# Kernel optimization log

Measured on AMD Instinct MI355X. Metric: run time of the kernel, lower is better.

Reference implementation:

```python
import jax, jax.numpy as jnp
import numpy as np

L, D, HQ, HKV, HD, P, V, B, S = 4, 2048, 16, 4, 128, 8192, 32000, 2, 1024
THETA, EPS = 500000.0, 1e-5
RATIO = HQ // HKV  # GQA q-to-kv ratio = 4


def rmsnorm(x, w):
    # torch: w * (x * rsqrt(mean(x^2, -1) + eps)) computed in fp32
    x32 = x.astype(jnp.float32)
    n = x32 * jax.lax.rsqrt(jnp.mean(x32 * x32, axis=-1, keepdims=True) + EPS)
    return w * n.astype(x.dtype)


def make_rope(seq_len):
    inv = 1.0 / (THETA ** (jnp.arange(0, HD, 2, dtype=jnp.float32) / HD))  # [HD/2]
    ang = jnp.arange(seq_len, dtype=jnp.float32)[:, None] * inv[None, :]   # [S, HD/2]
    return jnp.cos(ang)[None, :, None, :], jnp.sin(ang)[None, :, None, :]  # [1,S,1,HD/2]


def rope(t, cos, sin):
    # torch code: complex = t[..., :HD/2] + i*t[..., HD/2:], multiply by e^{i*ang},
    # then view_as_real + flatten -> INTERLEAVED (r0,i0,r1,i1,...) output layout.
    h = HD // 2
    r, im = t[..., :h], t[..., h:]
    orr = r * cos - im * sin
    oim = r * sin + im * cos
    return jnp.stack([orr, oim], axis=-1).reshape(t.shape)


def attention(x, wqkv, wo, cos, sin):
    b, s, _ = x.shape
    qkv = x @ wqkv                               # [b,s,D+2*HKV*HD]
    q = qkv[..., :D].reshape(b, s, HQ, HD)
    k = qkv[..., D:D + HKV * HD].reshape(b, s, HKV, HD)
    v = qkv[..., D + HKV * HD:].reshape(b, s, HKV, HD)
    q = rope(q, cos, sin)
    k = rope(k, cos, sin)
    # GQA: repeat_interleave kv heads to match q heads (offset=0 prefill; cache is identity)
    k = jnp.repeat(k, RATIO, axis=2)
    v = jnp.repeat(v, RATIO, axis=2)
    scale = 1.0 / np.sqrt(HD)
    scores = jnp.einsum('bqhd,bkhd->bhqk', q, k) * scale
    causal = jnp.tril(jnp.ones((s, s), dtype=bool))
    scores = jnp.where(causal[None, None], scores, jnp.finfo(scores.dtype).min)
    probs = jax.nn.softmax(scores, axis=-1)
    out = jnp.einsum('bhqk,bkhd->bqhd', probs, v).reshape(b, s, D)
    return out @ wo


def swiglu(x, wgu, wd):
    gu = x @ wgu                                  # [b,s,2P]
    gate, up = gu[..., :P], gu[..., P:]
    return (jax.nn.silu(gate) * up) @ wd


def setup_inputs() -> dict:
    key = jax.random.key(0)
    ks = jax.random.split(key, 8)
    sc = 0.02
    return {
        'tokens': jax.random.randint(ks[0], (B, S), 0, V),
        'emb': jax.random.normal(ks[1], (V, D), jnp.float32) * sc,
        'w_qkv': jax.random.normal(ks[2], (L, D, D + 2 * HKV * HD), jnp.float32) * sc,
        'w_o': jax.random.normal(ks[3], (L, D, D), jnp.float32) * sc,
        'w_gate_up': jax.random.normal(ks[4], (L, D, 2 * P), jnp.float32) * sc,
        'w_down': jax.random.normal(ks[5], (L, P, D), jnp.float32) * sc,
        'ln_attn': jnp.ones((L, D), jnp.float32),
        'ln_ffn': jnp.ones((L, D), jnp.float32),
        'ln_f': jnp.ones((D,), jnp.float32),
        'w_lm': jax.random.normal(ks[6], (D, V), jnp.float32) * sc,
    }


def reference(tokens, emb, w_qkv, w_o, w_gate_up, w_down, ln_attn, ln_ffn, ln_f, w_lm):
    cos, sin = make_rope(S)
    x = emb[tokens]                               # [B,S,D]
    for l in range(L):
        x = x + attention(rmsnorm(x, ln_attn[l]), w_qkv[l], w_o[l], cos, sin)
        x = x + swiglu(rmsnorm(x, ln_ffn[l]), w_gate_up[l], w_down[l])
    return rmsnorm(x, ln_f) @ w_lm                # logits [B,S,V]
```

## Files before the change

kernel.cpp:

```cpp
#include <hip/hip_runtime.h>
#include <hip/hip_bf16.h>
#include <math.h>

#define S_LEN 1024
#define DIM   2048
#define NHQ   16
#define NHKV  4
#define HDIM  128
#define PDIM  8192
#define VOCAB 32000
#define NLAYER 4
#define NROWS (2 * S_LEN)

typedef __attribute__((ext_vector_type(4))) float f32x4;
typedef __attribute__((ext_vector_type(8))) short bf16x8;

__device__ __forceinline__ void gload_lds16(const void* g, void* l) {
  __builtin_amdgcn_global_load_lds(
      (const __attribute__((address_space(1))) unsigned int*)g,
      (__attribute__((address_space(3))) unsigned int*)l, 16, 0, 0);
}

#define FENCE() asm volatile("" ::: "memory")

__global__ __launch_bounds__(256) void k_embed(const int* __restrict__ tokens,
    const float* __restrict__ emb, float* __restrict__ x) {
  int row = blockIdx.x;
  int tok = tokens[row];
  const f32x4* src = (const f32x4*)(emb + (size_t)tok * DIM);
  f32x4* dst = (f32x4*)(x + (size_t)row * DIM);
  for (int i = threadIdx.x; i < DIM / 4; i += 256) dst[i] = src[i];
}

__global__ __launch_bounds__(256) void k_rmsnorm(const float* __restrict__ x,
    const float* __restrict__ w, __hip_bfloat16* __restrict__ out) {
  int row = blockIdx.x;
  const float* xr = x + (size_t)row * DIM;
  float ss = 0.f;
  for (int i = threadIdx.x; i < DIM; i += 256) { float v = xr[i]; ss += v * v; }
  for (int off = 32; off; off >>= 1) ss += __shfl_xor(ss, off);
  __shared__ float wsum[4];
  if ((threadIdx.x & 63) == 0) wsum[threadIdx.x >> 6] = ss;
  __syncthreads();
  float tot = wsum[0] + wsum[1] + wsum[2] + wsum[3];
  float r = rsqrtf(tot / (float)DIM + 1e-5f);
  __hip_bfloat16* orow = out + (size_t)row * DIM;
  for (int i = threadIdx.x; i < DIM; i += 256)
    orow[i] = __float2bfloat16(w[i] * (xr[i] * r));
}

__global__ __launch_bounds__(256) void k_wt(const float* __restrict__ W,
    __hip_bfloat16* __restrict__ WT, int K, int N) {
  __shared__ __hip_bfloat16 t[64][72];
  int k0 = blockIdx.y * 64, n0 = blockIdx.x * 64;
  int r = threadIdx.x >> 4;
  int c4 = (threadIdx.x & 15) * 4;
#pragma unroll
  for (int i = 0; i < 4; ++i) {
    int k = r + i * 16;
    f32x4 v = *(const f32x4*)(W + (size_t)(k0 + k) * N + n0 + c4);
#pragma unroll
    for (int j = 0; j < 4; ++j) t[c4 + j][k] = __float2bfloat16(v[j]);
  }
  __syncthreads();
  int n = threadIdx.x >> 2, kc = (threadIdx.x & 3) * 16;
  bf16x8* dst = (bf16x8*)(WT + (size_t)(n0 + n) * K + k0 + kc);
  dst[0] = *(const bf16x8*)&t[n][kc];
  dst[1] = *(const bf16x8*)&t[n][kc + 8];
}

__global__ __launch_bounds__(256) void k_wt_gu(const float* __restrict__ W,
    __hip_bfloat16* __restrict__ WT, int K, int N) {
  __shared__ __hip_bfloat16 t[64][72];
  int k0 = blockIdx.y * 64, n0 = blockIdx.x * 64;
  int r = threadIdx.x >> 4;
  int c4 = (threadIdx.x & 15) * 4;
  int nblk = (n0 + c4) >> 4;
  int jj   = (n0 + c4) & 15;
  int srcc = ((nblk & 1) ? PDIM : 0) + ((nblk >> 1) << 4) + jj;
#pragma unroll
  for (int i = 0; i < 4; ++i) {
    int k = r + i * 16;
    f32x4 v = *(const f32x4*)(W + (size_t)(k0 + k) * N + srcc);
#pragma unroll
    for (int j = 0; j < 4; ++j) t[c4 + j][k] = __float2bfloat16(v[j]);
  }
  __syncthreads();
  int n = threadIdx.x >> 2, kc = (threadIdx.x & 3) * 16;
  bf16x8* dst = (bf16x8*)(WT + (size_t)(n0 + n) * K + k0 + kc);
  dst[0] = *(const bf16x8*)&t[n][kc];
  dst[1] = *(const bf16x8*)&t[n][kc + 8];
}

template<int EPI>
__global__ __launch_bounds__(512) void k_gemm256(
    const __hip_bfloat16* __restrict__ A, const __hip_bfloat16* __restrict__ BT,
    void* __restrict__ Cv, int M, int N, int K) {
  __shared__ __hip_bfloat16 AsH[4][128][64];
  __shared__ __hip_bfloat16 BsH[4][128][64];
  const int NH = K >> 5;
  int tid = threadIdx.x;
  int bid = blockIdx.x;
  int mt = bid & 7, nt = bid >> 3;
  int bm = mt << 8, bn = nt << 8;
  int wave = tid >> 6, lane = tid & 63;
  int wm = wave >> 2, wn = wave & 3;
  int g = lane >> 4, c = lane & 15;
  f32x4 acc[8][4] = {};

  int pre  = (lane & 7) ^ (lane >> 3);
  int rOff = (lane >> 3) * 2 + (pre >> 2);
  int cOff = (pre & 3) * 8;

  auto stageA = [&](int S, int h) {
#pragma unroll
    for (int rd = 0; rd < 2; ++rd) {
      int seg = rd * 8 + wave;
      gload_lds16(A + (size_t)(bm + seg * 16 + rOff) * K + h * 32 + cOff,
                  &AsH[S][seg * 8 + (lane >> 3)][(lane & 7) * 8]);
    }
  };
  auto stageB = [&](int S, int h) {
#pragma unroll
    for (int rd = 0; rd < 2; ++rd) {
      int seg = rd * 8 + wave;
      gload_lds16(BT + (size_t)(bn + seg * 16 + rOff) * K + h * 32 + cOff,
                  &BsH[S][seg * 8 + (lane >> 3)][(lane & 7) * 8]);
    }
  };

  stageA(0, 0); stageB(0, 0);
  stageA(1, 1); stageB(1, 1);
  stageB(2, 2);
  asm volatile("s_waitcnt vmcnt(6)" ::: "memory");
  __builtin_amdgcn_s_barrier();
  FENCE();

  int lineA = wm * 64 + (c >> 1);
  int lineB = wn * 32 + (c >> 1);
  int slotE = ((((c & 1) << 2) | g) ^ (c >> 1)) * 8;

  for (int H = 0; H < NH; ++H) {
    int S = H & 3;
    bf16x8 af[8], bv[4];
#pragma unroll
    for (int mi = 0; mi < 8; ++mi)
      af[mi] = *(const bf16x8*)&AsH[S][lineA + mi * 8][slotE];
#pragma unroll
    for (int ni = 0; ni < 4; ++ni)
      bv[ni] = *(const bf16x8*)&BsH[S][lineB + ni * 8][slotE];
    FENCE();
    if (H + 2 < NH) stageA((H + 2) & 3, H + 2);
    if (H + 3 < NH) stageB((H + 3) & 3, H + 3);
    if (H + 4 <= NH)      { asm volatile("s_waitcnt vmcnt(6)" ::: "memory"); }
    else if (H + 3 == NH) { asm volatile("s_waitcnt vmcnt(4)" ::: "memory"); }
    else if (H + 2 == NH) { asm volatile("s_waitcnt vmcnt(0)" ::: "memory"); }
    __builtin_amdgcn_s_barrier();
    asm volatile("s_waitcnt lgkmcnt(0)" ::: "memory");
    __builtin_amdgcn_sched_barrier(0);
    __builtin_amdgcn_s_setprio(1);
#pragma unroll
    for (int mi = 0; mi < 8; ++mi)
#pragma unroll
      for (int ni = 0; ni < 4; ++ni)
        acc[mi][ni] = __builtin_amdgcn_mfma_f32_16x16x32_bf16(af[mi], bv[ni], acc[mi][ni], 0, 0, 0);
    __builtin_amdgcn_s_setprio(0);
    FENCE();
    __builtin_amdgcn_s_barrier();
    FENCE();
  }

  float* Cf = (float*)Cv;
  __hip_bfloat16* Cb = (__hip_bfloat16*)Cv;
  int row0 = bm + wm * 128, col0 = bn + wn * 64;
  if (EPI == 3) {
#pragma unroll
    for (int mi = 0; mi < 8; ++mi)
#pragma unroll
      for (int ni = 0; ni < 4; ni += 2)
#pragma unroll
        for (int r = 0; r < 4; ++r) {
          int row = row0 + mi * 16 + g * 4 + r;
          int hcol = ((col0 + ni * 16) >> 1) + c;
          float gate = acc[mi][ni][r], up = acc[mi][ni + 1][r];
          float sv = gate / (1.f + __expf(-gate)) * up;
          Cb[(size_t)row * PDIM + hcol] = __float2bfloat16(sv);
        }
  } else {
#pragma unroll
    for (int mi = 0; mi < 8; ++mi)
#pragma unroll
      for (int ni = 0; ni < 4; ++ni)
#pragma unroll
        for (int r = 0; r < 4; ++r) {
          int row = row0 + mi * 16 + g * 4 + r;
          int col = col0 + ni * 16 + c;
          size_t idx = (size_t)row * N + col;
          if (EPI == 0) Cf[idx] = acc[mi][ni][r];
          else if (EPI == 1) Cf[idx] += acc[mi][ni][r];
          else Cb[idx] = __float2bfloat16(acc[mi][ni][r]);
        }
  }
}

template<int EPI, int KSPLIT = 1>
__global__ __launch_bounds__(256) void k_gemm_bt(
    const __hip_bfloat16* __restrict__ A, const __hip_bfloat16* __restrict__ BT,
    void* __restrict__ Cv, int M, int N, int K) {
  __shared__ __hip_bfloat16 As[2][128][64];
  __shared__ __hip_bfloat16 Bs[2][128][64];
  int nm = M >> 7;
  int bid = blockIdx.x;
  int mt, nt;
  if (nm == 16) {
    int xcd = bid & 7;
    int seq = bid >> 3;
    mt = (xcd << 1) | (seq & 1);
    nt = seq >> 1;
  } else {
    mt = bid % nm;
    nt = bid / nm;
  }
  int bm = mt << 7, bn = nt << 7;
  const int Keff = K / KSPLIT;
  const int kbase = (KSPLIT > 1) ? (int)blockIdx.y * Keff : 0;
  int tid  = threadIdx.x;
  int wave = tid >> 6, lane = tid & 63;
  int wr = (wave >> 1) * 64, wc = (wave & 1) * 64;
  int g = lane >> 4, c = lane & 15;
  f32x4 acc[4][4] = {};

  auto stage = [&](int buf, int k0) {
#pragma unroll
    for (int i = 0; i < 4; ++i) {
      int ci = i * 256 + tid;
      int row = ci >> 3, pc = ci & 7;
      int jl = pc ^ (row & 7);
      gload_lds16(A + (size_t)(bm + row) * K + kbase + k0 + jl * 8, &As[buf][row][pc * 8]);
      gload_lds16(BT + (size_t)(bn + row) * K + kbase + k0 + jl * 8, &Bs[buf][row][pc * 8]);
    }
  };

  int ntiles = Keff >> 6;
  stage(0, 0);
  if (ntiles > 1) stage(1, 64);

  for (int t = 0; t < ntiles; ++t) {
    int cur = t & 1;
    if (t + 1 < ntiles) asm volatile("s_waitcnt vmcnt(8)" ::: "memory");
    else                asm volatile("s_waitcnt vmcnt(0)" ::: "memory");
    __builtin_amdgcn_s_barrier();
    FENCE();
    __builtin_amdgcn_sched_barrier(0);
#pragma unroll
    for (int kk = 0; kk < 2; ++kk) {
      bf16x8 af[4], bv[4];
#pragma unroll
      for (int mi = 0; mi < 4; ++mi) {
        int row = wr + mi * 16 + c;
        int ch = (kk * 4 + g) ^ (row & 7);
        af[mi] = *(const bf16x8*)&As[cur][row][ch * 8];
      }
#pragma unroll
      for (int ni = 0; ni < 4; ++ni) {
        int row = wc + ni * 16 + c;
        int ch = (kk * 4 + g) ^ (row & 7);
        bv[ni] = *(const bf16x8*)&Bs[cur][row][ch * 8];
      }
      __builtin_amdgcn_s_setprio(1);
#pragma unroll
      for (int mi = 0; mi < 4; ++mi)
#pragma unroll
        for (int ni = 0; ni < 4; ++ni)
          acc[mi][ni] = __builtin_amdgcn_mfma_f32_16x16x32_bf16(af[mi], bv[ni], acc[mi][ni], 0, 0, 0);
      __builtin_amdgcn_s_setprio(0);
    }
    FENCE();
    __builtin_amdgcn_s_barrier();
    FENCE();
    if (t + 2 < ntiles) stage(cur, (t + 2) << 6);
  }

  float* Cf = (float*)Cv;
  __hip_bfloat16* Cb = (__hip_bfloat16*)Cv;
#pragma unroll
  for (int mi = 0; mi < 4; ++mi)
#pragma unroll
    for (int ni = 0; ni < 4; ++ni)
#pragma unroll
      for (int r = 0; r < 4; ++r) {
        int row = bm + wr + mi * 16 + g * 4 + r;
        int col = bn + wc + ni * 16 + c;
        size_t idx = (size_t)row * N + col;
        if (EPI == 0) Cf[idx] = acc[mi][ni][r];
        else if (EPI == 1) Cf[idx] += acc[mi][ni][r];
        else if (EPI == 2) Cb[idx] = __float2bfloat16(acc[mi][ni][r]);
        else atomicAdd(&Cf[idx], acc[mi][ni][r]);
      }
}

template<int EPI>
__global__ __launch_bounds__(256) void k_gemm(
    const __hip_bfloat16* __restrict__ A, const float* __restrict__ Bw,
    void* __restrict__ Cv, int M, int N, int K) {
  __shared__ __hip_bfloat16 As[128][32];
  __shared__ __hip_bfloat16 Bs[128][40];
  int tid  = threadIdx.x;
  int bm = blockIdx.y * 128, bn = blockIdx.x * 128;
  int wave = tid >> 6, lane = tid & 63;
  int wr = (wave >> 1) * 64, wc = (wave & 1) * 64;
  int lrow = lane & 15, lk = (lane >> 4) * 8;
  f32x4 acc[4][4] = {};
  for (int k0 = 0; k0 < K; k0 += 32) {
#pragma unroll
    for (int i = 0; i < 2; ++i) {
      int L = i * 256 + tid;
      int row = L >> 2, koff = (L & 3) * 8;
      gload_lds16(A + (size_t)(bm + row) * K + k0 + koff, &As[row][koff]);
    }
#pragma unroll
    for (int i = 0; i < 4; ++i) {
      int L = i * 256 + tid;
      int kk = L >> 5;
      int c4 = (L & 31) * 4;
      f32x4 v = *(const f32x4*)(Bw + (size_t)(k0 + kk) * N + bn + c4);
#pragma unroll
      for (int j = 0; j < 4; ++j) Bs[c4 + j][kk] = __float2bfloat16(v[j]);
    }
    __syncthreads();
    bf16x8 af[4], bfr[4];
#pragma unroll
    for (int mi = 0; mi < 4; ++mi)
      af[mi] = *(const bf16x8*)(&As[wr + mi * 16 + lrow][lk]);
#pragma unroll
    for (int ni = 0; ni < 4; ++ni)
      bfr[ni] = *(const bf16x8*)(&Bs[wc + ni * 16 + lrow][lk]);
#pragma unroll
    for (int mi = 0; mi < 4; ++mi)
#pragma unroll
      for (int ni = 0; ni < 4; ++ni)
        acc[mi][ni] = __builtin_amdgcn_mfma_f32_16x16x32_bf16(af[mi], bfr[ni], acc[mi][ni], 0, 0, 0);
    __syncthreads();
  }
  float* Cf = (float*)Cv;
  __hip_bfloat16* Cb = (__hip_bfloat16*)Cv;
#pragma unroll
  for (int mi = 0; mi < 4; ++mi)
#pragma unroll
    for (int ni = 0; ni < 4; ++ni)
#pragma unroll
      for (int r = 0; r < 4; ++r) {
        int row = bm + wr + mi * 16 + ((lane >> 4) * 4 + r);
        int col = bn + wc + ni * 16 + (lane & 15);
        size_t idx = (size_t)row * N + col;
        if (EPI == 0) Cf[idx] = acc[mi][ni][r];
        else if (EPI == 1) Cf[idx] += acc[mi][ni][r];
        else Cb[idx] = __float2bfloat16(acc[mi][ni][r]);
      }
}

__global__ __launch_bounds__(256) void k_rope(const __hip_bfloat16* __restrict__ qkv,
    __hip_bfloat16* __restrict__ qr, __hip_bfloat16* __restrict__ kr,
    __hip_bfloat16* __restrict__ vt) {
  int rowid = blockIdx.x;
  int b = rowid >> 10, s = rowid & (S_LEN - 1);
  const __hip_bfloat16* src = qkv + (size_t)rowid * 3072;
  const float kInvLog = 0.20503692777f;
  const float scale = 0.08838834764831845f;
  __shared__ float cs[64], sn[64];
  if (threadIdx.x < 64) {
    float inv = expf(-(float)threadIdx.x * kInvLog);
    float a = (float)s * inv;
    sincosf(a, &sn[threadIdx.x], &cs[threadIdx.x]);
  }
  __syncthreads();
  for (int it = threadIdx.x; it < NHQ * 64; it += 256) {
    int h = it >> 6, i = it & 63;
    float re = __bfloat162float(src[h * HDIM + i]);
    float im = __bfloat162float(src[h * HDIM + 64 + i]);
    size_t dst = ((size_t)(b * NHQ + h) * S_LEN + s) * HDIM;
    qr[dst + 2 * i]     = __float2bfloat16((re * cs[i] - im * sn[i]) * scale);
    qr[dst + 2 * i + 1] = __float2bfloat16((re * sn[i] + im * cs[i]) * scale);
  }
  for (int it = threadIdx.x; it < NHKV * 64; it += 256) {
    int h = it >> 6, i = it & 63;
    float re = __bfloat162float(src[DIM + h * HDIM + i]);
    float im = __bfloat162float(src[DIM + h * HDIM + 64 + i]);
    size_t dst = ((size_t)(b * NHKV + h) * S_LEN + s) * HDIM;
    kr[dst + 2 * i]     = __float2bfloat16(re * cs[i] - im * sn[i]);
    kr[dst + 2 * i + 1] = __float2bfloat16(re * sn[i] + im * cs[i]);
  }
  for (int it = threadIdx.x; it < NHKV * HDIM; it += 256) {
    int h = it >> 7, d = it & 127;
    vt[(((size_t)b * NHKV + h) * HDIM + d) * S_LEN + s] = src[DIM + NHKV * HDIM + it];
  }
}

__global__ __launch_bounds__(256) void k_attn_mfma(
    const __hip_bfloat16* __restrict__ Q,
    const __hip_bfloat16* __restrict__ Kc,
    const __hip_bfloat16* __restrict__ VT,
    __hip_bfloat16* __restrict__ O) {
  __shared__ __hip_bfloat16 plds[4][16][40];
  int wave = threadIdx.x >> 6, lane = threadIdx.x & 63;
  int gw = blockIdx.x * 4 + wave;
  int qt = gw & 63;
  int bh = gw >> 6;
  int b = bh >> 4, h = bh & 15;
  int hk = h >> 2;
  int q0 = qt * 16;
  int g = lane >> 4, c = lane & 15;
  const __hip_bfloat16* Qb = Q + ((size_t)bh * S_LEN + q0) * HDIM;
  const __hip_bfloat16* Kb = Kc + (size_t)(b * NHKV + hk) * S_LEN * HDIM;
  const __hip_bfloat16* Vb = VT + (size_t)(b * NHKV + hk) * S_LEN * HDIM;

  bf16x8 qf[4];
#pragma unroll
  for (int cn = 0; cn < 4; ++cn)
    qf[cn] = *(const bf16x8*)(Qb + (size_t)c * HDIM + cn * 32 + g * 8);

  f32x4 po[8] = {};
  float m[4], l[4];
#pragma unroll
  for (int r = 0; r < 4; ++r) { m[r] = -1e30f; l[r] = 0.f; }

  int kvend = q0 + 16;
  for (int kv0 = 0; kv0 < kvend; kv0 += 32) {
    f32x4 s0 = {}, s1 = {};
#pragma unroll
    for (int cn = 0; cn < 4; ++cn) {
      bf16x8 k0f = *(const bf16x8*)(Kb + (size_t)(kv0 + c) * HDIM + cn * 32 + g * 8);
      bf16x8 k1f = *(const bf16x8*)(Kb + (size_t)(kv0 + 16 + c) * HDIM + cn * 32 + g * 8);
      s0 = __builtin_amdgcn_mfma_f32_16x16x32_bf16(qf[cn], k0f, s0, 0, 0, 0);
      s1 = __builtin_amdgcn_mfma_f32_16x16x32_bf16(qf[cn], k1f, s1, 0, 0, 0);
    }
    if (kv0 + 31 > q0) {
#pragma unroll
      for (int r = 0; r < 4; ++r) {
        int qrow = q0 + g * 4 + r;
        if (kv0 + c > qrow)      s0[r] = -1e30f;
        if (kv0 + 16 + c > qrow) s1[r] = -1e30f;
      }
    }
    float rm[4];
#pragma unroll
    for (int r = 0; r < 4; ++r) rm[r] = fmaxf(s0[r], s1[r]);
#pragma unroll
    for (int off = 1; off < 16; off <<= 1)
#pragma unroll
      for (int r = 0; r < 4; ++r) rm[r] = fmaxf(rm[r], __shfl_xor(rm[r], off));
    float p0[4], p1[4], rs[4];
#pragma unroll
    for (int r = 0; r < 4; ++r) {
      float mn = fmaxf(m[r], rm[r]);
      float corr = __expf(m[r] - mn);
      m[r] = mn;
      p0[r] = __expf(s0[r] - mn);
      p1[r] = __expf(s1[r] - mn);
      rs[r] = p0[r] + p1[r];
      l[r] *= corr;
#pragma unroll
      for (int t = 0; t < 8; ++t) po[t][r] *= corr;
    }
#pragma unroll
    for (int off = 1; off < 16; off <<= 1)
#pragma unroll
      for (int r = 0; r < 4; ++r) rs[r] += __shfl_xor(rs[r], off);
#pragma unroll
    for (int r = 0; r < 4; ++r) l[r] += rs[r];
#pragma unroll
    for (int r = 0; r < 4; ++r) {
      plds[wave][g * 4 + r][c]      = __float2bfloat16(p0[r]);
      plds[wave][g * 4 + r][16 + c] = __float2bfloat16(p1[r]);
    }
    bf16x8 pf = *(const bf16x8*)&plds[wave][c][g * 8];
#pragma unroll
    for (int t = 0; t < 8; ++t) {
      bf16x8 vf = *(const bf16x8*)(Vb + (size_t)(t * 16 + c) * S_LEN + kv0 + g * 8);
      po[t] = __builtin_amdgcn_mfma_f32_16x16x32_bf16(pf, vf, po[t], 0, 0, 0);
    }
  }
  float inv[4];
#pragma unroll
  for (int r = 0; r < 4; ++r) inv[r] = 1.f / l[r];
  __hip_bfloat16* ob = O + ((size_t)(b * S_LEN) + q0) * DIM + h * HDIM;
#pragma unroll
  for (int t = 0; t < 8; ++t)
#pragma unroll
    for (int r = 0; r < 4; ++r)
      ob[(size_t)(g * 4 + r) * DIM + t * 16 + c] = __float2bfloat16(po[t][r] * inv[r]);
}

extern "C" void kernel_launch(void* const* d_in, const int* in_sizes, int n_in,
                              void* d_out, int out_size, void* d_ws, size_t ws_size,
                              hipStream_t stream) {
  const int*   tokens    = (const int*)d_in[0];
  const float* emb       = (const float*)d_in[1];
  const float* w_qkv     = (const float*)d_in[2];
  const float* w_o       = (const float*)d_in[3];
  const float* w_gate_up = (const float*)d_in[4];
  const float* w_down    = (const float*)d_in[5];
  const float* ln_attn   = (const float*)d_in[6];
  const float* ln_ffn    = (const float*)d_in[7];
  const float* ln_f      = (const float*)d_in[8];
  const float* w_lm      = (const float*)d_in[9];
  float* out = (float*)d_out;

  char* ws = (char*)d_ws;
  float* x = (float*)ws;                    ws += (size_t)NROWS * DIM * 4;
  __hip_bfloat16* xn = (__hip_bfloat16*)ws; ws += (size_t)NROWS * DIM * 2;
  __hip_bfloat16* qkvb = (__hip_bfloat16*)ws; ws += (size_t)NROWS * 3072 * 2;
  __hip_bfloat16* qr = (__hip_bfloat16*)ws; ws += (size_t)2 * NHQ * S_LEN * HDIM * 2;
  __hip_bfloat16* kr = (__hip_bfloat16*)ws; ws += (size_t)2 * NHKV * S_LEN * HDIM * 2;
  __hip_bfloat16* vt = (__hip_bfloat16*)ws; ws += (size_t)2 * NHKV * S_LEN * HDIM * 2;
  __hip_bfloat16* ao = (__hip_bfloat16*)ws; ws += (size_t)NROWS * DIM * 2;
  __hip_bfloat16* hb = (__hip_bfloat16*)ws; ws += (size_t)NROWS * PDIM * 2;
  __hip_bfloat16* wbuf = (__hip_bfloat16*)ws;
  size_t need = (size_t)(ws - (char*)d_ws) + (size_t)VOCAB * DIM * 2;
  bool bf16w = ws_size >= need;

  k_embed<<<NROWS, 256, 0, stream>>>(tokens, emb, x);

  for (int l = 0; l < NLAYER; ++l) {
    k_rmsnorm<<<NROWS, 256, 0, stream>>>(x, ln_attn + (size_t)l * DIM, xn);
    if (bf16w) {
      k_wt<<<dim3(3072 / 64, DIM / 64), 256, 0, stream>>>(
          w_qkv + (size_t)l * DIM * 3072, wbuf, DIM, 3072);
      k_gemm_bt<2><<<(NROWS / 128) * (3072 / 128), 256, 0, stream>>>(
          xn, wbuf, qkvb, NROWS, 3072, DIM);
    } else {
      k_gemm<2><<<dim3(3072 / 128, NROWS / 128), 256, 0, stream>>>(
          xn, w_qkv + (size_t)l * DIM * 3072, qkvb, NROWS, 3072, DIM);
    }
    k_rope<<<NROWS, 256, 0, stream>>>(qkvb, qr, kr, vt);
    k_attn_mfma<<<(2 * NHQ * (S_LEN / 16)) / 4, 256, 0, stream>>>(qr, kr, vt, ao);
    if (bf16w) {
      k_wt<<<dim3(DIM / 64, DIM / 64), 256, 0, stream>>>(
          w_o + (size_t)l * DIM * DIM, wbuf, DIM, DIM);
      k_gemm_bt<4, 2><<<dim3((NROWS / 128) * (DIM / 128), 2), 256, 0, stream>>>(
          ao, wbuf, x, NROWS, DIM, DIM);
    } else {
      k_gemm<1><<<dim3(DIM / 128, NROWS / 128), 256, 0, stream>>>(
          ao, w_o + (size_t)l * DIM * DIM, x, NROWS, DIM, DIM);
    }
    k_rmsnorm<<<NROWS, 256, 0, stream>>>(x, ln_ffn + (size_t)l * DIM, xn);
    if (bf16w) {
      k_wt_gu<<<dim3(2 * PDIM / 64, DIM / 64), 256, 0, stream>>>(
          w_gate_up + (size_t)l * DIM * 2 * PDIM, wbuf, DIM, 2 * PDIM);
      k_gemm256<3><<<8 * (2 * PDIM / 256), 512, 0, stream>>>(
          xn, wbuf, hb, NROWS, 2 * PDIM, DIM);
    } else {
      k_gemm<2><<<dim3(2 * PDIM / 128, NROWS / 128), 256, 0, stream>>>(
          xn, w_gate_up + (size_t)l * DIM * 2 * PDIM, (void*)hb, NROWS, 2 * PDIM, DIM);
    }
    if (bf16w) {
      k_wt<<<dim3(DIM / 64, PDIM / 64), 256, 0, stream>>>(
          w_down + (size_t)l * PDIM * DIM, wbuf, PDIM, DIM);
      k_gemm_bt<4, 2><<<dim3((NROWS / 128) * (DIM / 128), 2), 256, 0, stream>>>(
          hb, wbuf, x, NROWS, DIM, PDIM);
    } else {
      k_gemm<1><<<dim3(DIM / 128, NROWS / 128), 256, 0, stream>>>(
          hb, w_down + (size_t)l * PDIM * DIM, x, NROWS, DIM, PDIM);
    }
  }

  k_rmsnorm<<<NROWS, 256, 0, stream>>>(x, ln_f, xn);
  if (bf16w) {
    k_wt<<<dim3(VOCAB / 64, DIM / 64), 256, 0, stream>>>(w_lm, wbuf, DIM, VOCAB);
    k_gemm256<0><<<8 * (VOCAB / 256), 512, 0, stream>>>(
        xn, wbuf, out, NROWS, VOCAB, DIM);
  } else {
    k_gemm<0><<<dim3(VOCAB / 128, NROWS / 128), 256, 0, stream>>>(
        xn, w_lm, out, NROWS, VOCAB, DIM);
  }
}
```

Before: 2.425 ms.

## Switch 256-tile GEMM to 32x32x16 MFMA with matching gate/up interleave

Replaces the 16x16x32 bf16 MFMA tiling in the 256x256 GEMM kernel with 32x32x16 MFMAs, using f32x16 accumulators, new LDS fragment addressing and a rewritten output epilogue. The gate/up weight transpose now interleaves in blocks of 32 columns instead of 16, so the fused SwiGLU epilogue can pair accumulators that sit in the same lane. Larger MFMA tiles halve the LDS fragment reads per FLOP and cut the instruction count. The cost is a more complex register and output mapping, and a risk of LDS bank conflicts with the new slot swizzle.

```diff
diff --git a/kernel.cpp b/kernel.cpp
--- a/kernel.cpp
+++ b/kernel.cpp
@@ -13,6 +13,7 @@
 #define NROWS (2 * S_LEN)
 
 typedef __attribute__((ext_vector_type(4))) float f32x4;
+typedef __attribute__((ext_vector_type(16))) float f32x16;
 typedef __attribute__((ext_vector_type(8))) short bf16x8;
 
 __device__ __forceinline__ void gload_lds16(const void* g, void* l) {
@@ -75,9 +76,9 @@
   int k0 = blockIdx.y * 64, n0 = blockIdx.x * 64;
   int r = threadIdx.x >> 4;
   int c4 = (threadIdx.x & 15) * 4;
-  int nblk = (n0 + c4) >> 4;
-  int jj   = (n0 + c4) & 15;
-  int srcc = ((nblk & 1) ? PDIM : 0) + ((nblk >> 1) << 4) + jj;
+  int nblk = (n0 + c4) >> 5;
+  int jj   = (n0 + c4) & 31;
+  int srcc = ((nblk & 1) ? PDIM : 0) + ((nblk >> 1) << 5) + jj;
 #pragma unroll
   for (int i = 0; i < 4; ++i) {
     int k = r + i * 16;
@@ -105,8 +106,7 @@
   int bm = mt << 8, bn = nt << 8;
   int wave = tid >> 6, lane = tid & 63;
   int wm = wave >> 2, wn = wave & 3;
-  int g = lane >> 4, c = lane & 15;
-  f32x4 acc[8][4] = {};
+  f32x16 acc[4][2] = {};
 
   int pre  = (lane & 7) ^ (lane >> 3);
   int rOff = (lane >> 3) * 2 + (pre >> 2);
@@ -136,19 +136,27 @@
   __builtin_amdgcn_s_barrier();
   FENCE();
 
-  int lineA = wm * 64 + (c >> 1);
-  int lineB = wn * 32 + (c >> 1);
-  int slotE = ((((c & 1) << 2) | g) ^ (c >> 1)) * 8;
+  int l31 = lane & 31;
+  int lhalf = lane >> 5;
+  int rowpar = lane & 1;
+  int lineOff = l31 >> 1;
+  int l7 = lineOff & 7;
+  int slotK[2];
+  slotK[0] = ((((rowpar << 2) | (0 + lhalf)) ^ l7)) * 8;
+  slotK[1] = ((((rowpar << 2) | (2 + lhalf)) ^ l7)) * 8;
 
   for (int H = 0; H < NH; ++H) {
     int S = H & 3;
-    bf16x8 af[8], bv[4];
-#pragma unroll
-    for (int mi = 0; mi < 8; ++mi)
-      af[mi] = *(const bf16x8*)&AsH[S][lineA + mi * 8][slotE];
-#pragma unroll
-    for (int ni = 0; ni < 4; ++ni)
-      bv[ni] = *(const bf16x8*)&BsH[S][lineB + ni * 8][slotE];
+    bf16x8 af[2][4], bv[2][2];
+#pragma unroll
+    for (int ks = 0; ks < 2; ++ks) {
+#pragma unroll
+      for (int mi = 0; mi < 4; ++mi)
+        af[ks][mi] = *(const bf16x8*)&AsH[S][wm * 64 + mi * 16 + lineOff][slotK[ks]];
+#pragma unroll
+      for (int nj = 0; nj < 2; ++nj)
+        bv[ks][nj] = *(const bf16x8*)&BsH[S][wn * 32 + nj * 16 + lineOff][slotK[ks]];
+    }
     FENCE();
     if (H + 2 < NH) stageA((H + 2) & 3, H + 2);
     if (H + 3 < NH) stageB((H + 3) & 3, H + 3);
@@ -160,10 +168,12 @@
     __builtin_amdgcn_sched_barrier(0);
     __builtin_amdgcn_s_setprio(1);
 #pragma unroll
-    for (int mi = 0; mi < 8; ++mi)
-#pragma unroll
-      for (int ni = 0; ni < 4; ++ni)
-        acc[mi][ni] = __builtin_amdgcn_mfma_f32_16x16x32_bf16(af[mi], bv[ni], acc[mi][ni], 0, 0, 0);
+    for (int mi = 0; mi < 4; ++mi)
+#pragma unroll
+      for (int nj = 0; nj < 2; ++nj) {
+        acc[mi][nj] = __builtin_amdgcn_mfma_f32_32x32x16_bf16(af[0][mi], bv[0][nj], acc[mi][nj], 0, 0, 0);
+        acc[mi][nj] = __builtin_amdgcn_mfma_f32_32x32x16_bf16(af[1][mi], bv[1][nj], acc[mi][nj], 0, 0, 0);
+      }
     __builtin_amdgcn_s_setprio(0);
     FENCE();
     __builtin_amdgcn_s_barrier();
@@ -174,31 +184,29 @@
   __hip_bfloat16* Cb = (__hip_bfloat16*)Cv;
   int row0 = bm + wm * 128, col0 = bn + wn * 64;
   if (EPI == 3) {
-#pragma unroll
-    for (int mi = 0; mi < 8; ++mi)
-#pragma unroll
-      for (int ni = 0; ni < 4; ni += 2)
-#pragma unroll
-        for (int r = 0; r < 4; ++r) {
-          int row = row0 + mi * 16 + g * 4 + r;
-          int hcol = ((col0 + ni * 16) >> 1) + c;
-          float gate = acc[mi][ni][r], up = acc[mi][ni + 1][r];
-          float sv = gate / (1.f + __expf(-gate)) * up;
-          Cb[(size_t)row * PDIM + hcol] = __float2bfloat16(sv);
-        }
+    int hcol = (col0 >> 1) + l31;
+#pragma unroll
+    for (int mi = 0; mi < 4; ++mi)
+#pragma unroll
+      for (int reg = 0; reg < 16; ++reg) {
+        int row = row0 + mi * 32 + ((reg >> 2) << 3) + (reg & 3) + (lhalf << 2);
+        float gate = acc[mi][0][reg], up = acc[mi][1][reg];
+        float sv = gate / (1.f + __expf(-gate)) * up;
+        Cb[(size_t)row * PDIM + hcol] = __float2bfloat16(sv);
+      }
   } else {
 #pragma unroll
-    for (int mi = 0; mi < 8; ++mi)
-#pragma unroll
-      for (int ni = 0; ni < 4; ++ni)
-#pragma unroll
-        for (int r = 0; r < 4; ++r) {
-          int row = row0 + mi * 16 + g * 4 + r;
-          int col = col0 + ni * 16 + c;
+    for (int mi = 0; mi < 4; ++mi)
+#pragma unroll
+      for (int nj = 0; nj < 2; ++nj)
+#pragma unroll
+        for (int reg = 0; reg < 16; ++reg) {
+          int row = row0 + mi * 32 + ((reg >> 2) << 3) + (reg & 3) + (lhalf << 2);
+          int col = col0 + nj * 32 + l31;
           size_t idx = (size_t)row * N + col;
-          if (EPI == 0) Cf[idx] = acc[mi][ni][r];
-          else if (EPI == 1) Cf[idx] += acc[mi][ni][r];
-          else Cb[idx] = __float2bfloat16(acc[mi][ni][r]);
+          if (EPI == 0) Cf[idx] = acc[mi][nj][reg];
+          else if (EPI == 1) Cf[idx] += acc[mi][nj][reg];
+          else Cb[idx] = __float2bfloat16(acc[mi][nj][reg]);
         }
   }
 }
```

Result: slower. 2.510 ms (+3.5%).
